# Optimization experiments

Measured on AMD Instinct MI355X. Metric: run time of the kernel, lower is better.

Reference implementation:

```python
import jax, jax.numpy as jnp
import numpy as np

N_WIRES = 12
N_LAYERS = 4
OUT_DIM = 8
BATCH = 4096
DIM = 2 ** N_WIRES

# ---- gate matrices (accept scalar or [B] angles; return [...,2,2] complex64) ----

def _rx(t):
    c = jnp.cos(t / 2).astype(jnp.complex64)
    js = (-1j * jnp.sin(t / 2)).astype(jnp.complex64)
    return jnp.stack([jnp.stack([c, js], -1), jnp.stack([js, c], -1)], -2)

def _ry(t):
    c = jnp.cos(t / 2).astype(jnp.complex64)
    s = jnp.sin(t / 2).astype(jnp.complex64)
    return jnp.stack([jnp.stack([c, -s], -1), jnp.stack([s, c], -1)], -2)

def _rz(t):
    em = jnp.exp(-0.5j * t.astype(jnp.complex64))
    ep = jnp.exp(0.5j * t.astype(jnp.complex64))
    z = jnp.zeros_like(em)
    return jnp.stack([jnp.stack([em, z], -1), jnp.stack([z, ep], -1)], -2)


def _apply1(state, U, wire):
    # state: [B, 2**n]; U: [2,2] or [B,2,2]; wire 0 = most significant (PennyLane order)
    B, dim = state.shape
    left = 2 ** wire
    right = dim // (2 * left)
    s = state.reshape(B, left, 2, right)
    if U.ndim == 2:
        U = jnp.broadcast_to(U, (B, 2, 2))
    s = jnp.einsum('bij,bajc->baic', U, s)
    return s.reshape(B, dim)


def _cnot(state, ctrl):
    # CNOT on adjacent wires [ctrl, ctrl+1]
    B, dim = state.shape
    left = 2 ** ctrl
    right = dim // (4 * left)
    s = state.reshape(B, left, 2, 2, right)
    s = jnp.concatenate([s[:, :, 0:1], jnp.flip(s[:, :, 1:2], axis=3)], axis=2)
    return s.reshape(B, dim)


# sign of PauliZ eigenvalue of wire i for every basis state: [OUT_DIM, 2**n]
_idx = np.arange(DIM)
_Z_SIGNS = np.stack([1.0 - 2.0 * ((_idx >> (N_WIRES - 1 - i)) & 1)
                     for i in range(OUT_DIM)]).astype(np.float32)


def setup_inputs() -> dict:
    key = jax.random.key(0)
    kx, kw = jax.random.split(key)
    x = jax.random.normal(kx, (BATCH, 2), dtype=jnp.float32)
    weights = jax.random.normal(kw, (N_LAYERS, N_WIRES, 3), dtype=jnp.float32)
    return {"x": x, "weights": weights}


def reference(x, weights):
    B = x.shape[0]
    state = jnp.zeros((B, DIM), dtype=jnp.complex64).at[:, 0].set(1.0)
    enc = [_rx(x[:, 0]) if i % 2 == 0 else _ry(x[:, 1]) for i in range(N_WIRES)]
    for layer in range(N_LAYERS):
        for i in range(N_WIRES):
            state = _apply1(state, enc[i], i)
        for i in range(N_WIRES):
            state = _apply1(state, _rx(weights[layer, i, 0]), i)
            state = _apply1(state, _ry(weights[layer, i, 1]), i)
            state = _apply1(state, _rz(weights[layer, i, 2]), i)
        for i in range(N_WIRES - 1):
            state = _cnot(state, i)
    probs = state.real ** 2 + state.imag ** 2  # [B, 2**n]
    expvals = probs @ jnp.asarray(_Z_SIGNS).T  # [B, OUT_DIM]
    return expvals * jnp.float32(np.pi)
```

## Files before the change

### kernel.cpp

```cpp
#include <hip/hip_runtime.h>
#include <math.h>

#define NW 12
#define NL 4
#define DIM 4096

typedef float v2f __attribute__((ext_vector_type(2)));

__device__ __forceinline__ v2f cmul(v2f a, v2f b){
    v2f d; d.x = a.x*b.x - a.y*b.y; d.y = a.x*b.y + a.y*b.x; return d;
}

__device__ __forceinline__ v2f cx_mul_re(v2f a, v2f u){
    v2f d;
    asm("v_pk_mul_f32 %0, %1, %2 op_sel_hi:[1,0]"
        : "=v"(d) : "v"(a), "v"(u));
    return d;
}
__device__ __forceinline__ v2f cx_fma_re(v2f a, v2f u, v2f acc){
    v2f d;
    asm("v_pk_fma_f32 %0, %1, %2, %3 op_sel_hi:[1,0,1]"
        : "=v"(d) : "v"(a), "v"(u), "v"(acc));
    return d;
}
__device__ __forceinline__ v2f cx_fma_im(v2f a, v2f u, v2f acc){
    v2f d;
    asm("v_pk_fma_f32 %0, %1, %2, %3 op_sel:[1,1,0] op_sel_hi:[0,1,1] neg_lo:[0,1,0]"
        : "=v"(d) : "v"(a), "v"(u), "v"(acc));
    return d;
}

struct alignas(16) G { v2f u00, u01, u10, u11; };

__device__ __forceinline__ void bflys(v2f s[16], const G& g, const int m){
    #pragma unroll
    for (int r = 0; r < 16; ++r) if (!(r & m)) {
        const v2f a = s[r], b = s[r|m];
        v2f na = cx_fma_im(a, g.u00, cx_mul_re(a, g.u00));
        na     = cx_fma_im(b, g.u01, cx_fma_re(b, g.u01, na));
        v2f nb = cx_fma_im(a, g.u10, cx_mul_re(a, g.u10));
        nb     = cx_fma_im(b, g.u11, cx_fma_re(b, g.u11, nb));
        s[r] = na; s[r|m] = nb;
    }
}
__device__ __forceinline__ void seg4(v2f s[16], const G* g4){
    bflys(s, g4[0], 8);
    bflys(s, g4[1], 4);
    bflys(s, g4[2], 2);
    bflys(s, g4[3], 1);
}

__global__ __launch_bounds__(256) void qnn_kernel(const float* __restrict__ x,
                                                  const float* __restrict__ w,
                                                  float* __restrict__ out)
{
    __shared__ v2f st[DIM + (DIM >> 4)];
    __shared__ G ug[NL * NW];
    __shared__ float sred[32];

    const int b = blockIdx.x;
    const int t = threadIdx.x;
    const int th = t >> 4, tl = t & 15;

    if (t < NL * NW) {
        const int wire = t % NW;
        const float ang = (wire & 1) ? x[b * 2 + 1] : x[b * 2 + 0];
        float se, ce;
        sincosf(0.5f * ang, &se, &ce);
        v2f E0, E1, E2, E3;
        if ((wire & 1) == 0) {
            E0 = (v2f){ce, 0.f};  E1 = (v2f){0.f, -se};
            E2 = (v2f){0.f, -se}; E3 = (v2f){ce, 0.f};
        } else {
            E0 = (v2f){ce, 0.f};  E1 = (v2f){-se, 0.f};
            E2 = (v2f){se, 0.f};  E3 = (v2f){ce, 0.f};
        }
        const float w0 = w[t * 3 + 0];
        const float w1 = w[t * 3 + 1];
        const float w2 = w[t * 3 + 2];
        float s0, c0; sincosf(0.5f * w0, &s0, &c0);
        const v2f rx00 = (v2f){c0, 0.f}, rx01 = (v2f){0.f, -s0};
        v2f A0 = cmul(rx00, E0) + cmul(rx01, E2);
        v2f A1 = cmul(rx00, E1) + cmul(rx01, E3);
        v2f A2 = cmul(rx01, E0) + cmul(rx00, E2);
        v2f A3 = cmul(rx01, E1) + cmul(rx00, E3);
        float s1, c1; sincosf(0.5f * w1, &s1, &c1);
        v2f B0 = c1*A0 - s1*A2;
        v2f B1 = c1*A1 - s1*A3;
        v2f B2 = s1*A0 + c1*A2;
        v2f B3 = s1*A1 + c1*A3;
        float s2, c2; sincosf(0.5f * w2, &s2, &c2);
        const v2f em = (v2f){c2, -s2}, ep = (v2f){c2, s2};
        G gg;
        gg.u00 = cmul(em, B0); gg.u01 = cmul(em, B1);
        gg.u10 = cmul(ep, B2); gg.u11 = cmul(ep, B3);
        ug[t] = gg;
    }
    __syncthreads();

    v2f s[16];
    {
        const int u = (t ^ (t >> 1)) & 255;
        v2f Pb = (v2f){1.f, 0.f};
        #pragma unroll
        for (int wq = 0; wq < 8; ++wq) {
            const int bit = (u >> (7 - wq)) & 1;
            Pb = cmul(Pb, bit ? ug[wq].u10 : ug[wq].u00);
        }
        v2f L2[4], T4[4];
        #pragma unroll
        for (int k = 0; k < 4; ++k) {
            L2[k] = cmul(((k >> 1) & 1) ? ug[8].u10  : ug[8].u00,
                         (k & 1)        ? ug[9].u10  : ug[9].u00);
            T4[k] = cmul(((k >> 1) & 1) ? ug[10].u10 : ug[10].u00,
                         (k & 1)        ? ug[11].u10 : ug[11].u00);
        }
        const int t0 = t & 1;
        #pragma unroll
        for (int j = 0; j < 16; ++j) {
            const int l0 = j ^ (j >> 1);
            const v2f Lsel = L2[((l0 >> 2) & 3) ^ (t0 ? 2 : 0)];
            s[j] = cmul(Pb, cmul(Lsel, T4[l0 & 3]));
        }
    }

    int pidx[16];
    #pragma unroll
    for (int r = 0; r < 16; ++r) {
        const int n = (t << 4) | r;
        const int g = n ^ (n >> 1);
        pidx[r] = g + (g >> 4);
    }

    for (int layer = 1; layer < NL; ++layer) {
        const int gbase = layer * NW;

        seg4(s, &ug[gbase + 8]);

        if (layer > 1) __syncthreads();
        #pragma unroll
        for (int r = 0; r < 16; ++r) st[17*t + r] = s[r];
        __syncthreads();
        #pragma unroll
        for (int r = 0; r < 16; ++r) s[r] = st[272*th + 17*r + tl];

        seg4(s, &ug[gbase + 4]);

        #pragma unroll
        for (int r = 0; r < 16; ++r) st[272*th + 17*r + tl] = s[r];
        __syncthreads();
        #pragma unroll
        for (int r = 0; r < 16; ++r) s[r] = st[272*r + t + th];

        seg4(s, &ug[gbase + 0]);

        if (layer < NL - 1) {
            #pragma unroll
            for (int r = 0; r < 16; ++r) st[272*r + t + th] = s[r];
            __syncthreads();
            #pragma unroll
            for (int r = 0; r < 16; ++r) s[r] = st[pidx[r]];
        }
    }

    float p[16];
    #pragma unroll
    for (int r = 0; r < 16; ++r) {
        const v2f q = s[r] * s[r];
        p[r] = q.x + q.y;
    }
    float s0[8], d0[8];
    #pragma unroll
    for (int k = 0; k < 8; ++k) { s0[k] = p[2*k] + p[2*k+1]; d0[k] = p[2*k] - p[2*k+1]; }
    float s1[4], ds1[4], dd1[4];
    #pragma unroll
    for (int k = 0; k < 4; ++k) {
        s1[k]  = s0[2*k] + s0[2*k+1];
        ds1[k] = s0[2*k] - s0[2*k+1];
        dd1[k] = d0[2*k] - d0[2*k+1];
    }
    const float A0 = (s1[0]  + s1[1])  - (s1[2]  + s1[3]);
    const float A1 = (s1[0]  - s1[1])  - (s1[2]  - s1[3]);
    const float A2 = (ds1[0] - ds1[1]) - (ds1[2] - ds1[3]);
    const float A3 = (dd1[0] - dd1[1]) - (dd1[2] - dd1[3]);

    float vals[8];
    vals[0] = A0; vals[1] = A1; vals[2] = A2; vals[3] = A3;
    const int t7 = (t >> 7) & 1, t6 = (t >> 6) & 1, t5 = (t >> 5) & 1, t4 = (t >> 4) & 1;
    vals[4] = t7            ? -A3 : A3;
    vals[5] = (t7^t6)       ? -A3 : A3;
    vals[6] = (t7^t6^t5)    ? -A3 : A3;
    vals[7] = (t7^t6^t5^t4) ? -A3 : A3;

    const int lane = t & 63, wv = t >> 6;
    #pragma unroll
    for (int i = 0; i < 8; ++i) {
        float v = vals[i];
        #pragma unroll
        for (int off = 32; off; off >>= 1) v += __shfl_xor(v, off, 64);
        if (lane == 0) sred[wv * 8 + i] = v;
    }
    __syncthreads();
    if (t < 8) {
        const float r = sred[t] + sred[8 + t] + sred[16 + t] + sred[24 + t];
        out[b * 8 + t] = r * 3.14159265358979323846f;
    }
}

extern "C" void kernel_launch(void* const* d_in, const int* in_sizes, int n_in,
                              void* d_out, int out_size, void* d_ws, size_t ws_size,
                              hipStream_t stream) {
    const float* x = (const float*)d_in[0];
    const float* w = (const float*)d_in[1];
    float* out = (float*)d_out;
    qnn_kernel<<<4096, 256, 0, stream>>>(x, w, out);
}
```

Before: 164.3 us.

## Store statevector in packed fp16 and skip final-layer gates on unmeasured wires

Result: slower. 366.2 us (+122.9%).

```diff
diff --git a/kernel.cpp b/kernel.cpp
--- a/kernel.cpp
+++ b/kernel.cpp
@@ -6,56 +6,58 @@
 #define DIM 4096
 
 typedef float v2f __attribute__((ext_vector_type(2)));
+typedef _Float16 h2 __attribute__((ext_vector_type(2)));
 
 __device__ __forceinline__ v2f cmul(v2f a, v2f b){
     v2f d; d.x = a.x*b.x - a.y*b.y; d.y = a.x*b.y + a.y*b.x; return d;
 }
 
-__device__ __forceinline__ v2f cx_mul_re(v2f a, v2f u){
-    v2f d;
-    asm("v_pk_mul_f32 %0, %1, %2 op_sel_hi:[1,0]"
+__device__ __forceinline__ h2 cx_mul_re(h2 a, h2 u){
+    h2 d;
+    asm("v_pk_mul_f16 %0, %1, %2 op_sel:[0,0] op_sel_hi:[1,0]"
         : "=v"(d) : "v"(a), "v"(u));
     return d;
 }
-__device__ __forceinline__ v2f cx_fma_re(v2f a, v2f u, v2f acc){
-    v2f d;
-    asm("v_pk_fma_f32 %0, %1, %2, %3 op_sel_hi:[1,0,1]"
+__device__ __forceinline__ h2 cx_fma_re(h2 a, h2 u, h2 acc){
+    h2 d;
+    asm("v_pk_fma_f16 %0, %1, %2, %3 op_sel:[0,0,0] op_sel_hi:[1,0,1]"
         : "=v"(d) : "v"(a), "v"(u), "v"(acc));
     return d;
 }
-__device__ __forceinline__ v2f cx_fma_im(v2f a, v2f u, v2f acc){
-    v2f d;
-    asm("v_pk_fma_f32 %0, %1, %2, %3 op_sel:[1,1,0] op_sel_hi:[0,1,1] neg_lo:[0,1,0]"
+__device__ __forceinline__ h2 cx_fma_im(h2 a, h2 u, h2 acc){
+    h2 d;
+    asm("v_pk_fma_f16 %0, %1, %2, %3 op_sel:[1,1,0] op_sel_hi:[0,1,1] neg_lo:[0,1,0]"
         : "=v"(d) : "v"(a), "v"(u), "v"(acc));
     return d;
 }
 
-struct alignas(16) G { v2f u00, u01, u10, u11; };
-
-__device__ __forceinline__ void bflys(v2f s[16], const G& g, const int m){
+struct alignas(16) G16 { h2 u00, u01, u10, u11; };
+
+__device__ __forceinline__ void bflys(h2 s[16], const G16& g, const int m){
+    const h2 u00 = g.u00, u01 = g.u01, u10 = g.u10, u11 = g.u11;
     #pragma unroll
     for (int r = 0; r < 16; ++r) if (!(r & m)) {
-        const v2f a = s[r], b = s[r|m];
-        v2f na = cx_fma_im(a, g.u00, cx_mul_re(a, g.u00));
-        na     = cx_fma_im(b, g.u01, cx_fma_re(b, g.u01, na));
-        v2f nb = cx_fma_im(a, g.u10, cx_mul_re(a, g.u10));
-        nb     = cx_fma_im(b, g.u11, cx_fma_re(b, g.u11, nb));
+        const h2 a = s[r], b = s[r|m];
+        h2 na = cx_fma_im(a, u00, cx_mul_re(a, u00));
+        na    = cx_fma_im(b, u01, cx_fma_re(b, u01, na));
+        h2 nb = cx_fma_im(a, u10, cx_mul_re(a, u10));
+        nb    = cx_fma_im(b, u11, cx_fma_re(b, u11, nb));
         s[r] = na; s[r|m] = nb;
     }
 }
-__device__ __forceinline__ void seg4(v2f s[16], const G* g4){
+__device__ __forceinline__ void seg4(h2 s[16], const G16* g4){
     bflys(s, g4[0], 8);
     bflys(s, g4[1], 4);
     bflys(s, g4[2], 2);
     bflys(s, g4[3], 1);
 }
 
-__global__ __launch_bounds__(256) void qnn_kernel(const float* __restrict__ x,
-                                                  const float* __restrict__ w,
-                                                  float* __restrict__ out)
+__global__ __launch_bounds__(256, 8) void qnn_kernel(const float* __restrict__ x,
+                                                     const float* __restrict__ w,
+                                                     float* __restrict__ out)
 {
-    __shared__ v2f st[DIM + (DIM >> 4)];
-    __shared__ G ug[NL * NW];
+    __shared__ h2 st[DIM + (DIM >> 4)];
+    __shared__ G16 ug[NL * NW];
     __shared__ float sred[32];
 
     const int b = blockIdx.x;
@@ -91,51 +93,95 @@
         v2f B3 = s1*A1 + c1*A3;
         float s2, c2; sincosf(0.5f * w2, &s2, &c2);
         const v2f em = (v2f){c2, -s2}, ep = (v2f){c2, s2};
-        G gg;
-        gg.u00 = cmul(em, B0); gg.u01 = cmul(em, B1);
-        gg.u10 = cmul(ep, B2); gg.u11 = cmul(ep, B3);
+        const v2f u00 = cmul(em, B0), u01 = cmul(em, B1);
+        const v2f u10 = cmul(ep, B2), u11 = cmul(ep, B3);
+        G16 gg;
+        gg.u00 = (h2){(_Float16)u00.x, (_Float16)u00.y};
+        gg.u01 = (h2){(_Float16)u01.x, (_Float16)u01.y};
+        gg.u10 = (h2){(_Float16)u10.x, (_Float16)u10.y};
+        gg.u11 = (h2){(_Float16)u11.x, (_Float16)u11.y};
         ug[t] = gg;
     }
     __syncthreads();
 
-    v2f s[16];
+    h2 s[16];
     {
+        v2f col[12];
         const int u = (t ^ (t >> 1)) & 255;
+        #pragma unroll
+        for (int wq = 0; wq < 12; ++wq) {
+            const int wire = wq;
+            const float ang = (wire & 1) ? x[b * 2 + 1] : x[b * 2 + 0];
+            float se, ce; sincosf(0.5f * ang, &se, &ce);
+            v2f E0, E2;
+            if ((wire & 1) == 0) { E0 = (v2f){ce, 0.f}; E2 = (v2f){0.f, -se}; }
+            else                 { E0 = (v2f){ce, 0.f}; E2 = (v2f){se, 0.f};  }
+            const float w0 = w[wq * 3 + 0];
+            const float w1 = w[wq * 3 + 1];
+            const float w2 = w[wq * 3 + 2];
+            float s0, c0; sincosf(0.5f * w0, &s0, &c0);
+            const v2f rx00 = (v2f){c0, 0.f}, rx01 = (v2f){0.f, -s0};
+            v2f A0c = cmul(rx00, E0) + cmul(rx01, E2);
+            v2f A2c = cmul(rx01, E0) + cmul(rx00, E2);
+            float s1, c1; sincosf(0.5f * w1, &s1, &c1);
+            v2f B0c = c1*A0c - s1*A2c;
+            v2f B2c = s1*A0c + c1*A2c;
+            float s2, c2; sincosf(0.5f * w2, &s2, &c2);
+            const v2f em = (v2f){c2, -s2}, ep = (v2f){c2, s2};
+            if (wq < 8) {
+                const int bit = (u >> (7 - wq)) & 1;
+                col[wq] = bit ? cmul(ep, B2c) : cmul(em, B0c);
+            } else {
+                col[wq]     = cmul(em, B0c);
+            }
+        }
+        v2f c10[4];
+        #pragma unroll
+        for (int wq = 8; wq < 12; ++wq) {
+            const int wire = wq;
+            const float ang = (wire & 1) ? x[b * 2 + 1] : x[b * 2 + 0];
+            float se, ce; sincosf(0.5f * ang, &se, &ce);
+            v2f E0, E2;
+            if ((wire & 1) == 0) { E0 = (v2f){ce, 0.f}; E2 = (v2f){0.f, -se}; }
+            else                 { E0 = (v2f){ce, 0.f}; E2 = (v2f){se, 0.f};  }
+            const float w0 = w[wq * 3 + 0];
+            const float w1 = w[wq * 3 + 1];
+            const float w2 = w[wq * 3 + 2];
+            float s0, c0; sincosf(0.5f * w0, &s0, &c0);
+            const v2f rx00 = (v2f){c0, 0.f}, rx01 = (v2f){0.f, -s0};
+            v2f A0c = cmul(rx00, E0) + cmul(rx01, E2);
+            v2f A2c = cmul(rx01, E0) + cmul(rx00, E2);
+            float s1, c1; sincosf(0.5f * w1, &s1, &c1);
+            v2f B2c = s1*A0c + c1*A2c;
+            float s2, c2; sincosf(0.5f * w2, &s2, &c2);
+            const v2f ep = (v2f){c2, s2};
+            c10[wq - 8] = cmul(ep, B2c);
+        }
         v2f Pb = (v2f){1.f, 0.f};
         #pragma unroll
-        for (int wq = 0; wq < 8; ++wq) {
-            const int bit = (u >> (7 - wq)) & 1;
-            Pb = cmul(Pb, bit ? ug[wq].u10 : ug[wq].u00);
-        }
+        for (int wq = 0; wq < 8; ++wq) Pb = cmul(Pb, col[wq]);
         v2f L2[4], T4[4];
         #pragma unroll
         for (int k = 0; k < 4; ++k) {
-            L2[k] = cmul(((k >> 1) & 1) ? ug[8].u10  : ug[8].u00,
-                         (k & 1)        ? ug[9].u10  : ug[9].u00);
-            T4[k] = cmul(((k >> 1) & 1) ? ug[10].u10 : ug[10].u00,
-                         (k & 1)        ? ug[11].u10 : ug[11].u00);
+            L2[k] = cmul(((k >> 1) & 1) ? c10[0] : col[8],
+                         (k & 1)        ? c10[1] : col[9]);
+            T4[k] = cmul(((k >> 1) & 1) ? c10[2] : col[10],
+                         (k & 1)        ? c10[3] : col[11]);
         }
         const int t0 = t & 1;
         #pragma unroll
         for (int j = 0; j < 16; ++j) {
             const int l0 = j ^ (j >> 1);
             const v2f Lsel = L2[((l0 >> 2) & 3) ^ (t0 ? 2 : 0)];
-            s[j] = cmul(Pb, cmul(Lsel, T4[l0 & 3]));
-        }
-    }
-
-    int pidx[16];
-    #pragma unroll
-    for (int r = 0; r < 16; ++r) {
-        const int n = (t << 4) | r;
-        const int g = n ^ (n >> 1);
-        pidx[r] = g + (g >> 4);
+            const v2f amp = cmul(Pb, cmul(Lsel, T4[l0 & 3]));
+            s[j] = (h2){(_Float16)amp.x, (_Float16)amp.y};
+        }
     }
 
     for (int layer = 1; layer < NL; ++layer) {
         const int gbase = layer * NW;
 
-        seg4(s, &ug[gbase + 8]);
+        if (layer < NL - 1) seg4(s, &ug[gbase + 8]);
 
         if (layer > 1) __syncthreads();
         #pragma unroll
@@ -159,15 +205,19 @@
             for (int r = 0; r < 16; ++r) st[272*r + t + th] = s[r];
             __syncthreads();
             #pragma unroll
-            for (int r = 0; r < 16; ++r) s[r] = st[pidx[r]];
+            for (int r = 0; r < 16; ++r) {
+                const int n = (t << 4) | r;
+                const int g = n ^ (n >> 1);
+                s[r] = st[g + (g >> 4)];
+            }
         }
     }
 
     float p[16];
     #pragma unroll
     for (int r = 0; r < 16; ++r) {
-        const v2f q = s[r] * s[r];
-        p[r] = q.x + q.y;
+        const float re = (float)s[r].x, im = (float)s[r].y;
+        p[r] = re*re + im*im;
     }
     float s0[8], d0[8];
     #pragma unroll
```
